# Kernel optimization log

Hardware: AMD Instinct MI355X
Metric: run time of the kernel (lower is better)

Reference implementation:

```python
import jax, jax.numpy as jnp
import numpy as np

C = 256
NUM_HEADS = 4
GROUPS = 8
EPS = 1e-5


def setup_inputs() -> dict:
    key = jax.random.key(0)
    ks = jax.random.split(key, 8)
    N, H, W = 4, 64, 64
    x = jax.random.normal(ks[0], (N, C, H, W), dtype=jnp.float32)
    mask = jnp.ones((N, 1, H, W), dtype=jnp.float32)
    norm_w = jax.random.normal(ks[1], (C,), dtype=jnp.float32) * 0.02 + 1.0
    norm_b = jax.random.normal(ks[2], (C,), dtype=jnp.float32) * 0.02
    qkv_w = jax.random.normal(ks[3], (3 * C, C), dtype=jnp.float32) * (1.0 / np.sqrt(C))
    qkv_b = jax.random.normal(ks[4], (3 * C,), dtype=jnp.float32) * 0.02
    proj_w = jax.random.normal(ks[5], (C, C), dtype=jnp.float32) * (1.0 / np.sqrt(C))
    proj_b = jax.random.normal(ks[6], (C,), dtype=jnp.float32) * 0.02
    return {"x": x, "mask": mask, "norm_w": norm_w, "norm_b": norm_b,
            "qkv_w": qkv_w, "qkv_b": qkv_b, "proj_w": proj_w, "proj_b": proj_b}


def _group_norm(x, w, b):
    # x: [N, C, H, W]; normalize within GROUPS groups over (C//G, H, W)
    N, Cc, H, W = x.shape
    xg = x.reshape(N, GROUPS, Cc // GROUPS, H, W)
    mean = xg.mean(axis=(2, 3, 4), keepdims=True)
    var = xg.var(axis=(2, 3, 4), keepdims=True)
    xg = (xg - mean) * jax.lax.rsqrt(var + EPS)
    x = xg.reshape(N, Cc, H, W)
    return x * w[None, :, None, None] + b[None, :, None, None]


def reference(x, mask, norm_w, norm_b, qkv_w, qkv_b, proj_w, proj_b):
    N, Cc, H, W = x.shape
    h = NUM_HEADS
    hd = Cc // h  # head dim
    x_norm = _group_norm(x, norm_w, norm_b)
    # 1x1 conv == channel matmul: [N, 3C, H, W]
    qkv = jnp.einsum('nchw,oc->nohw', x_norm, qkv_w) + qkv_b[None, :, None, None]
    q, k, v = jnp.split(qkv, 3, axis=1)
    # n (h c) y x -> n h (y x) c
    def to_heads(t):
        return t.reshape(N, h, hd, H * W).transpose(0, 1, 3, 2)
    q, k, v = to_heads(q), to_heads(k), to_heads(v)
    scale = hd ** (-0.5)
    scores = jnp.einsum('nhic,nhjc->nhij', q, k) * scale  # [N,h,HW,HW]
    probs = jax.nn.softmax(scores, axis=-1)
    out = jnp.einsum('nhij,nhjc->nhic', probs, v)  # [N,h,HW,hd]
    # n h (y x) c -> n (h c) y x
    out = out.transpose(0, 1, 3, 2).reshape(N, Cc, H, W)
    out = jnp.einsum('nchw,oc->nohw', out, proj_w) + proj_b[None, :, None, None]
    y = (x + out) * mask[:, :1, :, :]  # broadcast over C (== repeat)
    return (y, mask)
```

## Files before the change

kernel.cpp:

```cpp
#include <hip/hip_runtime.h>

#define HW 4096
#define EPSV 1e-5f
#define SCL (0.125f * 1.44269504088896341f)

typedef unsigned short u16;
typedef unsigned int u32;
typedef __attribute__((ext_vector_type(8))) short short8;
typedef __attribute__((ext_vector_type(4))) short short4v;
typedef __attribute__((ext_vector_type(4))) float f32x4;

#define MFMA_K32(a, b, c) __builtin_amdgcn_mfma_f32_16x16x32_bf16((a), (b), (c), 0, 0, 0)
#if __has_builtin(__builtin_amdgcn_mfma_f32_16x16x16bf16_1k)
#define MFMA_K16(a, b, c) __builtin_amdgcn_mfma_f32_16x16x16bf16_1k((a), (b), (c), 0, 0, 0)
#elif __has_builtin(__builtin_amdgcn_mfma_f32_16x16x16_bf16)
#define MFMA_K16(a, b, c) __builtin_amdgcn_mfma_f32_16x16x16_bf16((a), (b), (c), 0, 0, 0)
#else
#define MFMA_K16(a, b, c) (c)
#endif

#define GLDS(g, l) __builtin_amdgcn_global_load_lds( \
    (const __attribute__((address_space(1))) u16*)(g), \
    (__attribute__((address_space(3))) u16*)(l), 16, 0, 0)

__device__ __forceinline__ u16 f2b(float f) {
    u32 u = __float_as_uint(f);
    u32 r = (u + 0x7FFFu + ((u >> 16) & 1u)) >> 16;
    return (u16)r;
}

__global__ __launch_bounds__(256) void gn_partial(const float* __restrict__ x, float* __restrict__ ps) {
    int bid = blockIdx.x;
    const float4* base = (const float4*)x + (size_t)bid * 2048;
    int t = threadIdx.x;
    float s = 0.f, sq = 0.f;
    for (int i = t; i < 2048; i += 256) {
        float4 v = base[i];
        s += v.x + v.y + v.z + v.w;
        sq += v.x * v.x + v.y * v.y + v.z * v.z + v.w * v.w;
    }
    __shared__ float rs[256], rq[256];
    rs[t] = s; rq[t] = sq;
    __syncthreads();
    for (int o = 128; o > 0; o >>= 1) {
        if (t < o) { rs[t] += rs[t + o]; rq[t] += rq[t + o]; }
        __syncthreads();
    }
    if (t == 0) { ps[2 * bid] = rs[0]; ps[2 * bid + 1] = rq[0]; }
}

__global__ __launch_bounds__(64) void gn_final(const float* __restrict__ ps, float* __restrict__ stats) {
    int t = threadIdx.x;
    if (t < 32) {
        float s = 0.f, sq = 0.f;
        for (int i = 0; i < 16; i++) {
            s += ps[2 * (t * 16 + i)];
            sq += ps[2 * (t * 16 + i) + 1];
        }
        float mean = s * (1.f / 131072.f);
        float var = sq * (1.f / 131072.f) - mean * mean;
        stats[t] = mean;
        stats[32 + t] = rsqrtf(var + EPSV);
    }
}

__global__ __launch_bounds__(256) void wconv(const float* __restrict__ src, u16* __restrict__ dst, int nscaled) {
    int idx = blockIdx.x * 256 + threadIdx.x;
    int row = idx >> 6;
    float sc = (row < nscaled) ? SCL : 1.0f;
    float4 v = *((const float4*)src + idx);
    u32 lo = (u32)f2b(v.x * sc) | ((u32)f2b(v.y * sc) << 16);
    u32 hi = (u32)f2b(v.z * sc) | ((u32)f2b(v.w * sc) << 16);
    uint2 o; o.x = lo; o.y = hi;
    *(uint2*)(dst + (size_t)idx * 4) = o;
}

__global__ __launch_bounds__(256) void gn_apply_t(const float* __restrict__ x, const float* __restrict__ w,
                                                  const float* __restrict__ b, const float* __restrict__ stats,
                                                  u16* __restrict__ xt) {
    __shared__ u16 Tt[64][72];
    int t = threadIdx.x;
    int p0 = blockIdx.x * 64;
    int c0 = blockIdx.y * 64;
    int n = blockIdx.z;
    int pc = (t & 15) * 4;
#pragma unroll
    for (int jj = 0; jj < 4; jj++) {
        int r = (t >> 4) + jj * 16;
        int c = c0 + r;
        int grp = n * 8 + (c >> 5);
        float mean = stats[grp], rstd = stats[32 + grp];
        float a = rstd * w[c];
        float bb = b[c] - mean * a;
        float4 v = *(const float4*)(x + ((size_t)n * 256 + c) * HW + p0 + pc);
        Tt[pc + 0][r] = f2b(v.x * a + bb);
        Tt[pc + 1][r] = f2b(v.y * a + bb);
        Tt[pc + 2][r] = f2b(v.z * a + bb);
        Tt[pc + 3][r] = f2b(v.w * a + bb);
    }
    __syncthreads();
    int p = t >> 2, ck = t & 3;
    short8 s0 = *(const short8*)&Tt[p][ck * 16];
    short8 s1 = *(const short8*)&Tt[p][ck * 16 + 8];
    u16* dst = xt + ((size_t)n * HW + p0 + p) * 256 + c0 + ck * 16;
    *(short8*)dst = s0;
    *(short8*)(dst + 8) = s1;
}

__global__ __launch_bounds__(256) void qkv_mfma(const u16* __restrict__ xt, const u16* __restrict__ Wb,
                                                const float* __restrict__ bq, u16* __restrict__ Qw,
                                                u16* __restrict__ Kw, u16* __restrict__ Vw) {
    __shared__ u16 Xs[64 * 256];
    int t = threadIdx.x;
    int w = t >> 6, lane = t & 63;
    int col = lane & 15, quad = lane >> 4;
    int p0 = blockIdx.x * 64;
    int o0 = blockIdx.y * 64;
    int n = blockIdx.z;

#pragma unroll
    for (int j = 0; j < 8; j++) {
        int rl = j * 2 + (lane >> 5);
        int row = w * 16 + rl;
        int slot = (lane & 31) ^ (rl & 7);
        GLDS(xt + ((size_t)n * HW + p0 + row) * 256 + slot * 8, Xs + (w * 16 + j * 2) * 256);
    }

    const u16* wrow = Wb + (size_t)(o0 + w * 16 + col) * 256 + quad * 8;
    short8 A[8];
#pragma unroll
    for (int ks = 0; ks < 8; ks++) A[ks] = *(const short8*)(wrow + ks * 32);

    __syncthreads();

    f32x4 C[4];
#pragma unroll
    for (int pb = 0; pb < 4; pb++) C[pb] = (f32x4){0.f, 0.f, 0.f, 0.f};
    int c7 = col & 7;
#pragma unroll
    for (int pb = 0; pb < 4; pb++) {
        const u16* xr = Xs + (pb * 16 + col) * 256;
#pragma unroll
        for (int ks = 0; ks < 8; ks++) {
            int slot = (ks * 4 + quad) ^ c7;
            short8 Bf = *(const short8*)(xr + slot * 8);
            C[pb] = MFMA_K32(A[ks], Bf, C[pb]);
        }
    }

    int type = o0 >> 8;
    int h = (o0 >> 6) & 3;
    int nh = n * 4 + h;
    float sc = (type == 0) ? SCL : 1.0f;
    if (type == 2) {
#pragma unroll
        for (int rg = 0; rg < 4; rg++) {
            int d = w * 16 + quad * 4 + rg;
            float bias = bq[o0 + d];
            u16* vb = Vw + ((size_t)nh * 64 + d) * HW + p0 + col;
#pragma unroll
            for (int pb = 0; pb < 4; pb++)
                vb[pb * 16] = f2b(C[pb][rg] + bias);
        }
    } else {
        u16* dst = (type == 0 ? Qw : Kw) + ((size_t)nh * HW + p0 + col) * 64 + w * 16 + quad * 4;
        float b0 = sc * bq[o0 + w * 16 + quad * 4 + 0];
        float b1 = sc * bq[o0 + w * 16 + quad * 4 + 1];
        float b2 = sc * bq[o0 + w * 16 + quad * 4 + 2];
        float b3 = sc * bq[o0 + w * 16 + quad * 4 + 3];
#pragma unroll
        for (int pb = 0; pb < 4; pb++) {
            uint2 o;
            o.x = (u32)f2b(C[pb][0] + b0) | ((u32)f2b(C[pb][1] + b1) << 16);
            o.y = (u32)f2b(C[pb][2] + b2) | ((u32)f2b(C[pb][3] + b3) << 16);
            *(uint2*)(dst + (size_t)(pb * 16) * 64) = o;
        }
    }
}

__global__ __launch_bounds__(512, 4) void flash_mfma(const u16* __restrict__ Qw, const u16* __restrict__ Kw,
                                                     const u16* __restrict__ Vw, u16* __restrict__ attnT) {
    __shared__ u16 Ks[4][64 * 64];
    __shared__ u16 Vts[4][64 * 64];
    int t = threadIdx.x;
    int w = t >> 6, lane = t & 63;
    int half = w >> 2, wl = w & 3;
    int col = lane & 15, quad = lane >> 4;
    int q0 = blockIdx.x * 128;
    int nh = blockIdx.y;

    const u16* qp = Qw + ((size_t)nh * HW + q0 + wl * 32 + col) * 64 + quad * 8;
    short8 qa0 = *(const short8*)qp;
    short8 qa1 = *(const short8*)(qp + 32);
    short8 qc0 = *(const short8*)(qp + 1024);
    short8 qc1 = *(const short8*)(qp + 1024 + 32);

    f32x4 OaA[4], OaB[4];
#pragma unroll
    for (int db = 0; db < 4; db++) {
        OaA[db] = (f32x4){0.f, 0.f, 0.f, 0.f};
        OaB[db] = (f32x4){0.f, 0.f, 0.f, 0.f};
    }
    f32x4 lacA = (f32x4){0.f, 0.f, 0.f, 0.f};
    f32x4 lacB = (f32x4){0.f, 0.f, 0.f, 0.f};

    const u16* kbase = Kw + (size_t)nh * HW * 64;
    const u16* vbase = Vw + (size_t)nh * 64 * HW;
    int lrK = lane >> 3;
    int ccK = lane & 7;
    size_t kSrc = (size_t)(wl * 8 + lrK) * 64 + (ccK ^ lrK) * 8;
    int jbase = half * 2048;

#define STAGE(jt_, b_) do { \
        int j0_ = jbase + (jt_) * 64; \
        _Pragma("unroll") \
        for (int s_ = 0; s_ < 2; s_++) \
            GLDS(kbase + (size_t)j0_ * 64 + kSrc + (size_t)(s_ * 32) * 64, &Ks[half * 2 + (b_)][(wl * 8 + s_ * 32) * 64]); \
        _Pragma("unroll") \
        for (int s_ = 0; s_ < 2; s_++) { \
            int d_ = wl * 8 + s_ * 32 + lrK; \
            GLDS(vbase + (size_t)d_ * HW + j0_ + ((ccK ^ lrK) * 8), &Vts[half * 2 + (b_)][(wl * 8 + s_ * 32) * 64]); \
        } \
    } while (0)

    STAGE(0, 0);
    __syncthreads();

    int c7 = col & 7;
    const short4v ones = {0x3F80, 0x3F80, 0x3F80, 0x3F80};
    for (int jt = 0; jt < 32; jt++) {
        int cur = jt & 1;
        if (jt < 31) STAGE(jt + 1, cur ^ 1);
        const u16* KsC = Ks[half * 2 + cur];
        const u16* VtC = Vts[half * 2 + cur];

        f32x4 sA[4], sB[4];
#pragma unroll
        for (int jb = 0; jb < 4; jb++) {
            const u16* kr = KsC + (jb * 16 + col) * 64;
            short8 ka0 = *(const short8*)(kr + ((quad ^ c7) * 8));
            short8 ka1 = *(const short8*)(kr + (((quad + 4) ^ c7) * 8));
            f32x4 a = (f32x4){0.f, 0.f, 0.f, 0.f};
            a = MFMA_K32(ka0, qa0, a);
            a = MFMA_K32(ka1, qa1, a);
            sA[jb] = a;
            f32x4 b = (f32x4){0.f, 0.f, 0.f, 0.f};
            b = MFMA_K32(ka0, qc0, b);
            b = MFMA_K32(ka1, qc1, b);
            sB[jb] = b;
        }

        short4v ptA[4], ptB[4];
#pragma unroll
        for (int jb = 0; jb < 4; jb++) {
            u32 ua[4], ub[4];
#pragma unroll
            for (int rg = 0; rg < 4; rg++) {
                ua[rg] = __float_as_uint(__builtin_amdgcn_exp2f(sA[jb][rg])) + 0x8000u;
                ub[rg] = __float_as_uint(__builtin_amdgcn_exp2f(sB[jb][rg])) + 0x8000u;
            }
            uint2 pa2, pb2;
            pa2.x = __builtin_amdgcn_perm(ua[1], ua[0], 0x07060302u);
            pa2.y = __builtin_amdgcn_perm(ua[3], ua[2], 0x07060302u);
            pb2.x = __builtin_amdgcn_perm(ub[1], ub[0], 0x07060302u);
            pb2.y = __builtin_amdgcn_perm(ub[3], ub[2], 0x07060302u);
            ptA[jb] = __builtin_bit_cast(short4v, pa2);
            ptB[jb] = __builtin_bit_cast(short4v, pb2);
        }

#pragma unroll
        for (int jb = 0; jb < 4; jb++) {
            lacA = MFMA_K16(ones, ptA[jb], lacA);
            lacB = MFMA_K16(ones, ptB[jb], lacB);
        }

#pragma unroll
        for (int db = 0; db < 4; db++) {
            const u16* vr = VtC + (db * 16 + col) * 64;
#pragma unroll
            for (int jb = 0; jb < 4; jb++) {
                int ch = jb * 2 + (quad >> 1);
                short4v va = *(const short4v*)(vr + ((ch ^ c7) * 8) + (quad & 1) * 4);
                OaA[db] = MFMA_K16(va, ptA[jb], OaA[db]);
                OaB[db] = MFMA_K16(va, ptB[jb], OaB[db]);
            }
        }
        __syncthreads();
    }
#undef STAGE

    float* mO = (float*)&Ks[0][0];
    float* mL = (float*)&Vts[0][0];
    int widx = wl * 64 + lane;
    if (half == 1) {
#pragma unroll
        for (int db = 0; db < 4; db++) {
#pragma unroll
            for (int rg = 0; rg < 4; rg++) {
                mO[(db * 8 + rg) * 256 + widx] = OaA[db][rg];
                mO[(db * 8 + 4 + rg) * 256 + widx] = OaB[db][rg];
            }
        }
        mL[widx] = lacA[0];
        mL[256 + widx] = lacB[0];
    }
    __syncthreads();
    if (half == 0) {
        float lA = lacA[0] + mL[widx];
        float lB = lacB[0] + mL[256 + widx];
        float rlA = 1.0f / lA, rlB = 1.0f / lB;
        u16* abA = attnT + ((size_t)(nh >> 2) * HW + q0 + wl * 32 + col) * 256 + (nh & 3) * 64 + quad * 4;
        u16* abB = abA + 16 * 256;
#pragma unroll
        for (int db = 0; db < 4; db++) {
            float a0 = OaA[db][0] + mO[(db * 8 + 0) * 256 + widx];
            float a1 = OaA[db][1] + mO[(db * 8 + 1) * 256 + widx];
            float a2 = OaA[db][2] + mO[(db * 8 + 2) * 256 + widx];
            float a3 = OaA[db][3] + mO[(db * 8 + 3) * 256 + widx];
            float b0 = OaB[db][0] + mO[(db * 8 + 4) * 256 + widx];
            float b1 = OaB[db][1] + mO[(db * 8 + 5) * 256 + widx];
            float b2 = OaB[db][2] + mO[(db * 8 + 6) * 256 + widx];
            float b3 = OaB[db][3] + mO[(db * 8 + 7) * 256 + widx];
            uint2 oA, oB;
            oA.x = (u32)f2b(a0 * rlA) | ((u32)f2b(a1 * rlA) << 16);
            oA.y = (u32)f2b(a2 * rlA) | ((u32)f2b(a3 * rlA) << 16);
            oB.x = (u32)f2b(b0 * rlB) | ((u32)f2b(b1 * rlB) << 16);
            oB.y = (u32)f2b(b2 * rlB) | ((u32)f2b(b3 * rlB) << 16);
            *(uint2*)(abA + db * 16) = oA;
            *(uint2*)(abB + db * 16) = oB;
        }
    }
}

__global__ __launch_bounds__(256) void proj_mfma(const u16* __restrict__ attnT, const u16* __restrict__ Wpb,
                                                 const float* __restrict__ bp, const float* __restrict__ x,
                                                 const float* __restrict__ mask, float* __restrict__ out) {
    __shared__ u16 Xs[64 * 256];
    int t = threadIdx.x;
    int w = t >> 6, lane = t & 63;
    int col = lane & 15, quad = lane >> 4;
    int p0 = blockIdx.x * 64;
    int o0 = blockIdx.y * 64;
    int n = blockIdx.z;

#pragma unroll
    for (int j = 0; j < 8; j++) {
        int rl = j * 2 + (lane >> 5);
        int row = w * 16 + rl;
        int slot = (lane & 31) ^ (rl & 7);
        GLDS(attnT + ((size_t)n * HW + p0 + row) * 256 + slot * 8, Xs + (w * 16 + j * 2) * 256);
    }

    const u16* wrow = Wpb + (size_t)(o0 + w * 16 + col) * 256 + quad * 8;
    short8 A[8];
#pragma unroll
    for (int ks = 0; ks < 8; ks++) A[ks] = *(const short8*)(wrow + ks * 32);

    __syncthreads();

    f32x4 C[4];
#pragma unroll
    for (int pb = 0; pb < 4; pb++) C[pb] = (f32x4){0.f, 0.f, 0.f, 0.f};
    int c7 = col & 7;
#pragma unroll
    for (int pb = 0; pb < 4; pb++) {
        const u16* xr = Xs + (pb * 16 + col) * 256;
#pragma unroll
        for (int ks = 0; ks < 8; ks++) {
            int slot = (ks * 4 + quad) ^ c7;
            short8 Bf = *(const short8*)(xr + slot * 8);
            C[pb] = MFMA_K32(A[ks], Bf, C[pb]);
        }
    }

#pragma unroll
    for (int rg = 0; rg < 4; rg++) {
        int o = o0 + w * 16 + quad * 4 + rg;
        float bias = bp[o];
        const float* xb = x + ((size_t)n * 256 + o) * HW + p0 + col;
        float* ob = out + ((size_t)n * 256 + o) * HW + p0 + col;
        const float* mb = mask + (size_t)n * HW + p0 + col;
#pragma unroll
        for (int pb = 0; pb < 4; pb++) {
            float mv = mb[pb * 16];
            ob[pb * 16] = (xb[pb * 16] + C[pb][rg] + bias) * mv;
        }
    }
}

__global__ __launch_bounds__(256) void mask_copy(const float* __restrict__ mask, float* __restrict__ out) {
    int i = blockIdx.x * 256 + threadIdx.x;
    out[i] = mask[i];
}

extern "C" void kernel_launch(void* const* d_in, const int* in_sizes, int n_in,
                              void* d_out, int out_size, void* d_ws, size_t ws_size,
                              hipStream_t stream) {
    const float* x = (const float*)d_in[0];
    const float* mask = (const float*)d_in[1];
    const float* norm_w = (const float*)d_in[2];
    const float* norm_b = (const float*)d_in[3];
    const float* qkv_w = (const float*)d_in[4];
    const float* qkv_b = (const float*)d_in[5];
    const float* proj_w = (const float*)d_in[6];
    const float* proj_b = (const float*)d_in[7];
    float* out = (float*)d_out;

    float* ws = (float*)d_ws;
    float* stats = ws;
    float* pstats = ws + 64;
    u16* xt = (u16*)(ws + 2048);
    u16* Qw = xt + 4194304;
    u16* Kw = Qw + 4194304;
    u16* Vw = Kw + 4194304;
    u16* attnT = Vw + 4194304;
    u16* Wqb = attnT + 4194304;
    u16* Wpb = Wqb + 196608;

    gn_partial<<<512, 256, 0, stream>>>(x, pstats);
    gn_final<<<1, 64, 0, stream>>>(pstats, stats);
    wconv<<<192, 256, 0, stream>>>(qkv_w, Wqb, 256);
    wconv<<<64, 256, 0, stream>>>(proj_w, Wpb, 0);
    gn_apply_t<<<dim3(64, 4, 4), 256, 0, stream>>>(x, norm_w, norm_b, stats, xt);
    qkv_mfma<<<dim3(64, 12, 4), 256, 0, stream>>>(xt, Wqb, qkv_b, Qw, Kw, Vw);
    flash_mfma<<<dim3(32, 16), 512, 0, stream>>>(Qw, Kw, Vw, attnT);
    proj_mfma<<<dim3(64, 4, 4), 256, 0, stream>>>(attnT, Wpb, proj_b, x, mask, out);
    mask_copy<<<64, 256, 0, stream>>>(mask, out + 4194304);
}
```

Measured before the change: 211.0 us.

## Load K tiles directly into registers and interleave score/exp phases

K tiles are no longer staged through LDS; each lane loads its K fragments from global memory straight into registers and prefetches the next tile in the middle of the iteration. Only V goes through LDS now, which halves the shared-memory footprint and LDS read traffic. The A and B score computations are also split so exp work for one half overlaps MFMA for the other. The trade-off is higher register pressure and every wave of a half issuing redundant global K loads, which now rely on the cache.

```diff
diff --git a/kernel.cpp b/kernel.cpp
--- a/kernel.cpp
+++ b/kernel.cpp
@@ -180,8 +180,7 @@
 
 __global__ __launch_bounds__(512, 4) void flash_mfma(const u16* __restrict__ Qw, const u16* __restrict__ Kw,
                                                      const u16* __restrict__ Vw, u16* __restrict__ attnT) {
-    __shared__ u16 Ks[4][64 * 64];
-    __shared__ u16 Vts[4][64 * 64];
+    __shared__ u16 smem[4 * 4096 + 1024];
     int t = threadIdx.x;
     int w = t >> 6, lane = t & 63;
     int half = w >> 2, wl = w & 3;
@@ -204,22 +203,27 @@
     f32x4 lacA = (f32x4){0.f, 0.f, 0.f, 0.f};
     f32x4 lacB = (f32x4){0.f, 0.f, 0.f, 0.f};
 
-    const u16* kbase = Kw + (size_t)nh * HW * 64;
     const u16* vbase = Vw + (size_t)nh * 64 * HW;
     int lrK = lane >> 3;
     int ccK = lane & 7;
-    size_t kSrc = (size_t)(wl * 8 + lrK) * 64 + (ccK ^ lrK) * 8;
     int jbase = half * 2048;
+
+    const u16* kp = Kw + (size_t)nh * HW * 64 + (size_t)jbase * 64 + col * 64 + quad * 8;
+    short8 kc[4][2];
+#pragma unroll
+    for (int jb = 0; jb < 4; jb++) {
+        kc[jb][0] = *(const short8*)(kp + jb * 1024);
+        kc[jb][1] = *(const short8*)(kp + jb * 1024 + 32);
+    }
+    kp += 4096;
 
 #define STAGE(jt_, b_) do { \
         int j0_ = jbase + (jt_) * 64; \
         _Pragma("unroll") \
-        for (int s_ = 0; s_ < 2; s_++) \
-            GLDS(kbase + (size_t)j0_ * 64 + kSrc + (size_t)(s_ * 32) * 64, &Ks[half * 2 + (b_)][(wl * 8 + s_ * 32) * 64]); \
-        _Pragma("unroll") \
         for (int s_ = 0; s_ < 2; s_++) { \
             int d_ = wl * 8 + s_ * 32 + lrK; \
-            GLDS(vbase + (size_t)d_ * HW + j0_ + ((ccK ^ lrK) * 8), &Vts[half * 2 + (b_)][(wl * 8 + s_ * 32) * 64]); \
+            GLDS(vbase + (size_t)d_ * HW + j0_ + ((ccK ^ lrK) * 8), \
+                 smem + (half * 2 + (b_)) * 4096 + (wl * 8 + s_ * 32) * 64); \
         } \
     } while (0)
 
@@ -231,40 +235,57 @@
     for (int jt = 0; jt < 32; jt++) {
         int cur = jt & 1;
         if (jt < 31) STAGE(jt + 1, cur ^ 1);
-        const u16* KsC = Ks[half * 2 + cur];
-        const u16* VtC = Vts[half * 2 + cur];
-
-        f32x4 sA[4], sB[4];
+        const u16* VtC = smem + (half * 2 + cur) * 4096;
+
+        f32x4 sA[4];
 #pragma unroll
         for (int jb = 0; jb < 4; jb++) {
-            const u16* kr = KsC + (jb * 16 + col) * 64;
-            short8 ka0 = *(const short8*)(kr + ((quad ^ c7) * 8));
-            short8 ka1 = *(const short8*)(kr + (((quad + 4) ^ c7) * 8));
             f32x4 a = (f32x4){0.f, 0.f, 0.f, 0.f};
-            a = MFMA_K32(ka0, qa0, a);
-            a = MFMA_K32(ka1, qa1, a);
+            a = MFMA_K32(kc[jb][0], qa0, a);
+            a = MFMA_K32(kc[jb][1], qa1, a);
             sA[jb] = a;
-            f32x4 b = (f32x4){0.f, 0.f, 0.f, 0.f};
-            b = MFMA_K32(ka0, qc0, b);
-            b = MFMA_K32(ka1, qc1, b);
-            sB[jb] = b;
-        }
-
-        short4v ptA[4], ptB[4];
+        }
+        short4v ptA[4];
 #pragma unroll
         for (int jb = 0; jb < 4; jb++) {
-            u32 ua[4], ub[4];
-#pragma unroll
-            for (int rg = 0; rg < 4; rg++) {
+            u32 ua[4];
+#pragma unroll
+            for (int rg = 0; rg < 4; rg++)
                 ua[rg] = __float_as_uint(__builtin_amdgcn_exp2f(sA[jb][rg])) + 0x8000u;
-                ub[rg] = __float_as_uint(__builtin_amdgcn_exp2f(sB[jb][rg])) + 0x8000u;
-            }
-            uint2 pa2, pb2;
+            uint2 pa2;
             pa2.x = __builtin_amdgcn_perm(ua[1], ua[0], 0x07060302u);
             pa2.y = __builtin_amdgcn_perm(ua[3], ua[2], 0x07060302u);
+            ptA[jb] = __builtin_bit_cast(short4v, pa2);
+        }
+
+        f32x4 sB[4];
+#pragma unroll
+        for (int jb = 0; jb < 4; jb++) {
+            f32x4 b = (f32x4){0.f, 0.f, 0.f, 0.f};
+            b = MFMA_K32(kc[jb][0], qc0, b);
+            b = MFMA_K32(kc[jb][1], qc1, b);
+            sB[jb] = b;
+        }
+
+        if (jt < 31) {
+#pragma unroll
+            for (int jb = 0; jb < 4; jb++) {
+                kc[jb][0] = *(const short8*)(kp + jb * 1024);
+                kc[jb][1] = *(const short8*)(kp + jb * 1024 + 32);
+            }
+            kp += 4096;
+        }
+
+        short4v ptB[4];
+#pragma unroll
+        for (int jb = 0; jb < 4; jb++) {
+            u32 ub[4];
+#pragma unroll
+            for (int rg = 0; rg < 4; rg++)
+                ub[rg] = __float_as_uint(__builtin_amdgcn_exp2f(sB[jb][rg])) + 0x8000u;
+            uint2 pb2;
             pb2.x = __builtin_amdgcn_perm(ub[1], ub[0], 0x07060302u);
             pb2.y = __builtin_amdgcn_perm(ub[3], ub[2], 0x07060302u);
-            ptA[jb] = __builtin_bit_cast(short4v, pa2);
             ptB[jb] = __builtin_bit_cast(short4v, pb2);
         }
 
@@ -289,8 +310,8 @@
     }
 #undef STAGE
 
-    float* mO = (float*)&Ks[0][0];
-    float* mL = (float*)&Vts[0][0];
+    float* mO = (float*)smem;
+    float* mL = (float*)(smem + 16384);
     int widx = wl * 64 + lane;
     if (half == 1) {
 #pragma unroll
```

After: 261.8 us. 24.0% more time.

## Fuse small prep kernels and loop output tiles inside QKV/proj GEMM blocks

Applied to the files above, without the earlier changes.

Folds the mask copy into gn_partial and merges gn_final with both weight conversions into one prep kernel, cutting four launches down to two. The QKV and projection GEMMs now have each block keep its staged activation tile in LDS and loop over all output-channel tiles, prefetching the next weight fragment into registers. This removes redundant global loads of the activation tile. The trade-off is far fewer blocks (256 instead of 3072/1024) and more serial work per block, which may reduce parallelism and latency hiding.

```diff
diff --git a/kernel.cpp b/kernel.cpp
--- a/kernel.cpp
+++ b/kernel.cpp
@@ -29,10 +29,14 @@
     return (u16)r;
 }
 
-__global__ __launch_bounds__(256) void gn_partial(const float* __restrict__ x, float* __restrict__ ps) {
+__global__ __launch_bounds__(256) void gn_partial(const float* __restrict__ x, float* __restrict__ ps,
+                                                  const float* __restrict__ mask, float* __restrict__ outm) {
     int bid = blockIdx.x;
+    int t = threadIdx.x;
+    if (bid < 16) {
+        ((float4*)outm)[bid * 256 + t] = ((const float4*)mask)[bid * 256 + t];
+    }
     const float4* base = (const float4*)x + (size_t)bid * 2048;
-    int t = threadIdx.x;
     float s = 0.f, sq = 0.f;
     for (int i = t; i < 2048; i += 256) {
         float4 v = base[i];
@@ -49,23 +53,28 @@
     if (t == 0) { ps[2 * bid] = rs[0]; ps[2 * bid + 1] = rq[0]; }
 }
 
-__global__ __launch_bounds__(64) void gn_final(const float* __restrict__ ps, float* __restrict__ stats) {
-    int t = threadIdx.x;
-    if (t < 32) {
-        float s = 0.f, sq = 0.f;
-        for (int i = 0; i < 16; i++) {
-            s += ps[2 * (t * 16 + i)];
-            sq += ps[2 * (t * 16 + i) + 1];
-        }
-        float mean = s * (1.f / 131072.f);
-        float var = sq * (1.f / 131072.f) - mean * mean;
-        stats[t] = mean;
-        stats[32 + t] = rsqrtf(var + EPSV);
-    }
-}
-
-__global__ __launch_bounds__(256) void wconv(const float* __restrict__ src, u16* __restrict__ dst, int nscaled) {
-    int idx = blockIdx.x * 256 + threadIdx.x;
+__global__ __launch_bounds__(256) void prep(const float* __restrict__ ps, float* __restrict__ stats,
+                                            const float* __restrict__ qkv_w, u16* __restrict__ Wqb,
+                                            const float* __restrict__ proj_w, u16* __restrict__ Wpb) {
+    int bid = blockIdx.x;
+    int t = threadIdx.x;
+    if (bid == 0) {
+        if (t < 32) {
+            float s = 0.f, sq = 0.f;
+            for (int i = 0; i < 16; i++) {
+                s += ps[2 * (t * 16 + i)];
+                sq += ps[2 * (t * 16 + i) + 1];
+            }
+            float mean = s * (1.f / 131072.f);
+            float var = sq * (1.f / 131072.f) - mean * mean;
+            stats[t] = mean;
+            stats[32 + t] = rsqrtf(var + EPSV);
+        }
+        return;
+    }
+    const float* src; u16* dst; int nscaled; int idx;
+    if (bid <= 192) { src = qkv_w; dst = Wqb; nscaled = 256; idx = (bid - 1) * 256 + t; }
+    else            { src = proj_w; dst = Wpb; nscaled = 0;   idx = (bid - 193) * 256 + t; }
     int row = idx >> 6;
     float sc = (row < nscaled) ? SCL : 1.0f;
     float4 v = *((const float4*)src + idx);
@@ -115,7 +124,6 @@
     int w = t >> 6, lane = t & 63;
     int col = lane & 15, quad = lane >> 4;
     int p0 = blockIdx.x * 64;
-    int o0 = blockIdx.y * 64;
     int n = blockIdx.z;
 
 #pragma unroll
@@ -126,55 +134,67 @@
         GLDS(xt + ((size_t)n * HW + p0 + row) * 256 + slot * 8, Xs + (w * 16 + j * 2) * 256);
     }
 
-    const u16* wrow = Wb + (size_t)(o0 + w * 16 + col) * 256 + quad * 8;
+    const u16* wrow = Wb + (size_t)(w * 16 + col) * 256 + quad * 8;
     short8 A[8];
 #pragma unroll
     for (int ks = 0; ks < 8; ks++) A[ks] = *(const short8*)(wrow + ks * 32);
 
     __syncthreads();
 
-    f32x4 C[4];
-#pragma unroll
-    for (int pb = 0; pb < 4; pb++) C[pb] = (f32x4){0.f, 0.f, 0.f, 0.f};
     int c7 = col & 7;
-#pragma unroll
-    for (int pb = 0; pb < 4; pb++) {
-        const u16* xr = Xs + (pb * 16 + col) * 256;
-#pragma unroll
-        for (int ks = 0; ks < 8; ks++) {
-            int slot = (ks * 4 + quad) ^ c7;
-            short8 Bf = *(const short8*)(xr + slot * 8);
-            C[pb] = MFMA_K32(A[ks], Bf, C[pb]);
-        }
-    }
-
-    int type = o0 >> 8;
-    int h = (o0 >> 6) & 3;
-    int nh = n * 4 + h;
-    float sc = (type == 0) ? SCL : 1.0f;
-    if (type == 2) {
-#pragma unroll
-        for (int rg = 0; rg < 4; rg++) {
-            int d = w * 16 + quad * 4 + rg;
-            float bias = bq[o0 + d];
-            u16* vb = Vw + ((size_t)nh * 64 + d) * HW + p0 + col;
-#pragma unroll
-            for (int pb = 0; pb < 4; pb++)
-                vb[pb * 16] = f2b(C[pb][rg] + bias);
-        }
-    } else {
-        u16* dst = (type == 0 ? Qw : Kw) + ((size_t)nh * HW + p0 + col) * 64 + w * 16 + quad * 4;
-        float b0 = sc * bq[o0 + w * 16 + quad * 4 + 0];
-        float b1 = sc * bq[o0 + w * 16 + quad * 4 + 1];
-        float b2 = sc * bq[o0 + w * 16 + quad * 4 + 2];
-        float b3 = sc * bq[o0 + w * 16 + quad * 4 + 3];
+    for (int ot = 0; ot < 12; ot++) {
+        int o0 = ot * 64;
+        short8 An[8];
+        if (ot < 11) {
+            const u16* wn = wrow + (size_t)(o0 + 64) * 256;
+#pragma unroll
+            for (int ks = 0; ks < 8; ks++) An[ks] = *(const short8*)(wn + ks * 32);
+        }
+
+        f32x4 C[4];
+#pragma unroll
+        for (int pb = 0; pb < 4; pb++) C[pb] = (f32x4){0.f, 0.f, 0.f, 0.f};
 #pragma unroll
         for (int pb = 0; pb < 4; pb++) {
-            uint2 o;
-            o.x = (u32)f2b(C[pb][0] + b0) | ((u32)f2b(C[pb][1] + b1) << 16);
-            o.y = (u32)f2b(C[pb][2] + b2) | ((u32)f2b(C[pb][3] + b3) << 16);
-            *(uint2*)(dst + (size_t)(pb * 16) * 64) = o;
-        }
+            const u16* xr = Xs + (pb * 16 + col) * 256;
+#pragma unroll
+            for (int ks = 0; ks < 8; ks++) {
+                int slot = (ks * 4 + quad) ^ c7;
+                short8 Bf = *(const short8*)(xr + slot * 8);
+                C[pb] = MFMA_K32(A[ks], Bf, C[pb]);
+            }
+        }
+
+        int type = o0 >> 8;
+        int h = (o0 >> 6) & 3;
+        int nh = n * 4 + h;
+        float sc = (type == 0) ? SCL : 1.0f;
+        if (type == 2) {
+#pragma unroll
+            for (int rg = 0; rg < 4; rg++) {
+                int d = w * 16 + quad * 4 + rg;
+                float bias = bq[o0 + d];
+                u16* vb = Vw + ((size_t)nh * 64 + d) * HW + p0 + col;
+#pragma unroll
+                for (int pb = 0; pb < 4; pb++)
+                    vb[pb * 16] = f2b(C[pb][rg] + bias);
+            }
+        } else {
+            u16* dst = (type == 0 ? Qw : Kw) + ((size_t)nh * HW + p0 + col) * 64 + w * 16 + quad * 4;
+            float b0 = sc * bq[o0 + w * 16 + quad * 4 + 0];
+            float b1 = sc * bq[o0 + w * 16 + quad * 4 + 1];
+            float b2 = sc * bq[o0 + w * 16 + quad * 4 + 2];
+            float b3 = sc * bq[o0 + w * 16 + quad * 4 + 3];
+#pragma unroll
+            for (int pb = 0; pb < 4; pb++) {
+                uint2 o;
+                o.x = (u32)f2b(C[pb][0] + b0) | ((u32)f2b(C[pb][1] + b1) << 16);
+                o.y = (u32)f2b(C[pb][2] + b2) | ((u32)f2b(C[pb][3] + b3) << 16);
+                *(uint2*)(dst + (size_t)(pb * 16) * 64) = o;
+            }
+        }
+#pragma unroll
+        for (int ks = 0; ks < 8; ks++) A[ks] = An[ks];
     }
 }
 
@@ -340,7 +360,6 @@
     int w = t >> 6, lane = t & 63;
     int col = lane & 15, quad = lane >> 4;
     int p0 = blockIdx.x * 64;
-    int o0 = blockIdx.y * 64;
     int n = blockIdx.z;
 
 #pragma unroll
@@ -351,46 +370,53 @@
         GLDS(attnT + ((size_t)n * HW + p0 + row) * 256 + slot * 8, Xs + (w * 16 + j * 2) * 256);
     }
 
-    const u16* wrow = Wpb + (size_t)(o0 + w * 16 + col) * 256 + quad * 8;
+    const u16* wrow = Wpb + (size_t)(w * 16 + col) * 256 + quad * 8;
     short8 A[8];
 #pragma unroll
     for (int ks = 0; ks < 8; ks++) A[ks] = *(const short8*)(wrow + ks * 32);
 
     __syncthreads();
 
-    f32x4 C[4];
-#pragma unroll
-    for (int pb = 0; pb < 4; pb++) C[pb] = (f32x4){0.f, 0.f, 0.f, 0.f};
     int c7 = col & 7;
-#pragma unroll
-    for (int pb = 0; pb < 4; pb++) {
-        const u16* xr = Xs + (pb * 16 + col) * 256;
-#pragma unroll
-        for (int ks = 0; ks < 8; ks++) {
-            int slot = (ks * 4 + quad) ^ c7;
-            short8 Bf = *(const short8*)(xr + slot * 8);
-            C[pb] = MFMA_K32(A[ks], Bf, C[pb]);
-        }
-    }
-
-#pragma unroll
-    for (int rg = 0; rg < 4; rg++) {
-        int o = o0 + w * 16 + quad * 4 + rg;
-        float bias = bp[o];
-        const float* xb = x + ((size_t)n * 256 + o) * HW + p0 + col;
-        float* ob = out + ((size_t)n * 256 + o) * HW + p0 + col;
-        const float* mb = mask + (size_t)n * HW + p0 + col;
+    for (int ot = 0; ot < 4; ot++) {
+        int o0 = ot * 64;
+        short8 An[8];
+        if (ot < 3) {
+            const u16* wn = wrow + (size_t)(o0 + 64) * 256;
+#pragma unroll
+            for (int ks = 0; ks < 8; ks++) An[ks] = *(const short8*)(wn + ks * 32);
+        }
+
+        f32x4 C[4];
+#pragma unroll
+        for (int pb = 0; pb < 4; pb++) C[pb] = (f32x4){0.f, 0.f, 0.f, 0.f};
 #pragma unroll
         for (int pb = 0; pb < 4; pb++) {
-            float mv = mb[pb * 16];
-            ob[pb * 16] = (xb[pb * 16] + C[pb][rg] + bias) * mv;
-        }
-    }
-}
-
-__global__ __launch_bounds__(256) void mask_copy(const float* __restrict__ mask, float* __restrict__ out) {
-    int i = blockIdx.x * 256 + threadIdx.x;
-    out[i] = mask[i];
+            const u16* xr = Xs + (pb * 16 + col) * 256;
+#pragma unroll
+            for (int ks = 0; ks < 8; ks++) {
+                int slot = (ks * 4 + quad) ^ c7;
+                short8 Bf = *(const short8*)(xr + slot * 8);
+                C[pb] = MFMA_K32(A[ks], Bf, C[pb]);
+            }
+        }
+
+#pragma unroll
+        for (int rg = 0; rg < 4; rg++) {
+            int o = o0 + w * 16 + quad * 4 + rg;
+            float bias = bp[o];
+            const float* xb = x + ((size_t)n * 256 + o) * HW + p0 + col;
+            float* ob = out + ((size_t)n * 256 + o) * HW + p0 + col;
+            const float* mb = mask + (size_t)n * HW + p0 + col;
+#pragma unroll
+            for (int pb = 0; pb < 4; pb++) {
+                float mv = mb[pb * 16];
+                ob[pb * 16] = (xb[pb * 16] + C[pb][rg] + bias) * mv;
+            }
+        }
+#pragma unroll
+        for (int ks = 0; ks < 8; ks++) A[ks] = An[ks];
+    }
 }
 
 extern "C" void kernel_launch(void* const* d_in, const int* in_sizes, int n_in,
@@ -417,13 +443,10 @@
     u16* Wqb = attnT + 4194304;
     u16* Wpb = Wqb + 196608;
 
-    gn_partial<<<512, 256, 0, stream>>>(x, pstats);
-    gn_final<<<1, 64, 0, stream>>>(pstats, stats);
-    wconv<<<192, 256, 0, stream>>>(qkv_w, Wqb, 256);
-    wconv<<<64, 256, 0, stream>>>(proj_w, Wpb, 0);
+    gn_partial<<<512, 256, 0, stream>>>(x, pstats, mask, out + 4194304);
+    prep<<<257, 256, 0, stream>>>(pstats, stats, qkv_w, Wqb, proj_w, Wpb);
     gn_apply_t<<<dim3(64, 4, 4), 256, 0, stream>>>(x, norm_w, norm_b, stats, xt);
-    qkv_mfma<<<dim3(64, 12, 4), 256, 0, stream>>>(xt, Wqb, qkv_b, Qw, Kw, Vw);
+    qkv_mfma<<<dim3(64, 1, 4), 256, 0, stream>>>(xt, Wqb, qkv_b, Qw, Kw, Vw);
     flash_mfma<<<dim3(32, 16), 512, 0, stream>>>(Qw, Kw, Vw, attnT);
-    proj_mfma<<<dim3(64, 4, 4), 256, 0, stream>>>(attnT, Wpb, proj_b, x, mask, out);
-    mask_copy<<<64, 256, 0, stream>>>(mask, out + 4194304);
-}
+    proj_mfma<<<dim3(64, 1, 4), 256, 0, stream>>>(attnT, Wpb, proj_b, x, mask, out);
+}
```

After: 217.6 us. 1.03x slower.
